# Performance work log

Hardware: AMD Instinct MI355X
Metric: run time of the kernel (lower is better)

Reference implementation:

```python
import jax, jax.numpy as jnp
import numpy as np

N_EMB = 512
DIM = 64
BETA = 0.25
EPS = 1e-10


def setup_inputs() -> dict:
    key = jax.random.key(0)
    k1, k2 = jax.random.split(key)
    z = jax.random.normal(k1, (32, 64, 64, 64), dtype=jnp.float32)  # (B, C=DIM, H, W)
    # embedding weight initialized uniform(-1/K, 1/K) as in the module
    weight = jax.random.uniform(k2, (N_EMB, DIM), dtype=jnp.float32,
                                minval=-1.0 / N_EMB, maxval=1.0 / N_EMB)
    return {"z": z, "weight": weight}


def reference(z, weight):
    # (B,C,H,W) -> (B,H,W,C)
    zp = jnp.transpose(z, (0, 2, 3, 1))
    zf = zp.reshape(-1, DIM)  # (N, D)
    # pairwise squared distances ||z||^2 + ||e||^2 - 2 z.e  -> (N, K)
    d = (jnp.sum(zf * zf, axis=1, keepdims=True)
         + jnp.sum(weight * weight, axis=1)
         - 2.0 * zf @ weight.T)
    codebook = jnp.argmin(d, axis=1)  # (N,)
    encodings = jax.nn.one_hot(codebook, N_EMB, dtype=zf.dtype)  # (N, K)
    # direct gather == one_hot @ weight (same math, efficient form)
    z_q = weight[codebook].reshape(zp.shape)
    sg = jax.lax.stop_gradient
    loss = jnp.mean((sg(z_q) - zp) ** 2) + BETA * jnp.mean((z_q - sg(zp)) ** 2)
    # straight-through estimator
    z_q = zp + sg(z_q - zp)
    e_mean = jnp.mean(encodings, axis=0)
    perplexity = jnp.exp(-jnp.sum(e_mean * jnp.log(e_mean + EPS)))
    z_q = jnp.transpose(z_q, (0, 3, 1, 2))  # back to (B,C,H,W)
    return (loss, z_q, perplexity, encodings, codebook)
```

## Files before the change

### kernel.cpp

```cpp
#include <hip/hip_runtime.h>
#include <math.h>

#define NK 512
#define NPTS (32*64*64)
#define NELEM (32*64*64*64)

#define OFF_LOSS 0
#define OFF_ZQ   1
#define OFF_PERP (1 + NELEM)
#define OFF_ENC  (2 + NELEM)
#define OFF_CB   (2 + NELEM + (size_t)NPTS * NK)


__global__ __launch_bounds__(256) void vq_prep(const float* __restrict__ wg,
                                               float* __restrict__ wT,
                                               float* __restrict__ bnd) {
    __shared__ float tl[64 * 65];
    const int t = threadIdx.x;
    const int kbase = blockIdx.x * 64;
    #pragma unroll
    for (int it = 0; it < 16; ++it) {
        int i = it * 256 + t;
        int k = i >> 6, d = i & 63;
        tl[k * 65 + d] = wg[(size_t)(kbase + k) * 64 + d];
    }
    __syncthreads();
    #pragma unroll
    for (int it = 0; it < 16; ++it) {
        int j = it * 256 + t;
        int d = j >> 6, kk = j & 63;
        wT[(size_t)d * 512 + kbase + kk] = tl[kk * 65 + d];
    }
    if (t < 64) {
        float s = 0.f;
        #pragma unroll 4
        for (int d = 0; d < 64; ++d) {
            float v = tl[t * 65 + d];
            s = __fadd_rn(s, __fmul_rn(v, v));
        }
        bnd[kbase + t] = s;
    }
}

__global__ __launch_bounds__(256, 2) void vq_main(const float* __restrict__ zg,
                                                  const float* __restrict__ wg,
                                                  const float* __restrict__ wT,
                                                  const float* __restrict__ bndg,
                                                  float* __restrict__ out,
                                                  int* __restrict__ hist,
                                                  double* __restrict__ lossAcc) {
    const int t = threadIdx.x;
    const int blk = blockIdx.x;
    const int b = blk >> 6;
    const int h = blk & 63;

    __shared__ __align__(16) float zt[64 * 64];
    __shared__ __align__(16) float wt[64 * 256];

    float* aRow = wt;
    float* redv = wt;
    int*   redi = (int*)(wt + 2048);
    float* zqt  = wt + 4096;
    int*   idxs = (int*)(wt + 8192);
    float* wsum = wt + 8256;

    {
        const int w = t & 63;
        const int c0 = t >> 6;
        const size_t base = (size_t)b * 262144 + (size_t)h * 64;
        #pragma unroll
        for (int c = c0; c < 64; c += 4)
            zt[c * 64 + w] = zg[base + (size_t)c * 4096 + w];
    }
    __syncthreads();

    if (t < 64) {
        float s = 0.f;
        for (int d = 0; d < 64; ++d) {
            float v = zt[d * 64 + t];
            s = __fadd_rn(s, __fmul_rn(v, v));
        }
        aRow[t] = s;
    }
    __syncthreads();

    const int tx = t & 7;
    const int ty = t >> 3;
    const int p0 = tx * 8;
    const int k0 = ty * 8;

    float av[8];
    {
        float4 a0 = *(const float4*)(aRow + p0);
        float4 a1 = *(const float4*)(aRow + p0 + 4);
        av[0] = a0.x; av[1] = a0.y; av[2] = a0.z; av[3] = a0.w;
        av[4] = a1.x; av[5] = a1.y; av[6] = a1.z; av[7] = a1.w;
    }
    __syncthreads();

    float best[8];
    int bidx[8];
    #pragma unroll
    for (int i = 0; i < 8; ++i) { best[i] = INFINITY; bidx[i] = 0; }

    const float4* wT4 = (const float4*)wT;
    float4* wt4 = (float4*)wt;

    for (int c = 0; c < 2; ++c) {
        if (c) __syncthreads();

        #pragma unroll
        for (int it = 0; it < 16; ++it) {
            int i = it * 256 + t;
            int d = i >> 6, c4 = i & 63;
            wt4[d * 64 + c4] = wT4[(size_t)d * 128 + c * 64 + c4];
        }

        float bn[8];
        {
            const float4* bp = (const float4*)(bndg + c * 256 + k0);
            float4 b0 = bp[0], b1 = bp[1];
            bn[0] = b0.x; bn[1] = b0.y; bn[2] = b0.z; bn[3] = b0.w;
            bn[4] = b1.x; bn[5] = b1.y; bn[6] = b1.z; bn[7] = b1.w;
        }
        __syncthreads();

        float acc[8][8];
        #pragma unroll
        for (int i = 0; i < 8; ++i)
            #pragma unroll
            for (int j = 0; j < 8; ++j) acc[i][j] = 0.f;

        const float* ztp = zt + p0;
        const float* wtp = wt + k0;
        #pragma unroll 4
        for (int d = 0; d < 64; ++d) {
            float4 z0 = *(const float4*)(ztp + d * 64);
            float4 z1 = *(const float4*)(ztp + d * 64 + 4);
            float4 w0 = *(const float4*)(wtp + d * 256);
            float4 w1 = *(const float4*)(wtp + d * 256 + 4);
            const float zr[8] = {z0.x, z0.y, z0.z, z0.w, z1.x, z1.y, z1.z, z1.w};
            const float wr[8] = {w0.x, w0.y, w0.z, w0.w, w1.x, w1.y, w1.z, w1.w};
            #pragma unroll
            for (int i = 0; i < 8; ++i)
                #pragma unroll
                for (int j = 0; j < 8; ++j)
                    acc[i][j] = fmaf(zr[i], wr[j], acc[i][j]);
        }

        #pragma unroll
        for (int i = 0; i < 8; ++i) {
            #pragma unroll
            for (int j = 0; j < 8; ++j) {
                float dist = __fsub_rn(__fadd_rn(av[i], bn[j]), 2.0f * acc[i][j]);
                int k = c * 256 + k0 + j;
                if (dist < best[i]) { best[i] = dist; bidx[i] = k; }
            }
        }
    }
    __syncthreads();

    #pragma unroll
    for (int i = 0; i < 8; ++i) {
        redv[ty * 64 + p0 + i] = best[i];
        redi[ty * 64 + p0 + i] = bidx[i];
    }
    __syncthreads();

    if (t < 64) {
        float bv = redv[t];
        int bi = redi[t];
        #pragma unroll
        for (int x = 1; x < 32; ++x) {
            float v = redv[x * 64 + t];
            int ii = redi[x * 64 + t];
            if (v < bv || (v == bv && ii < bi)) { bv = v; bi = ii; }
        }
        idxs[t] = bi;
        atomicAdd(&hist[bi], 1);
        out[OFF_CB + (size_t)blk * 64 + t] = (float)bi;
        const float4* wr4 = (const float4*)(wg + (size_t)bi * 64);
        #pragma unroll
        for (int q = 0; q < 16; ++q) {
            float4 v = wr4[q];
            zqt[(4 * q + 0) * 64 + t] = v.x;
            zqt[(4 * q + 1) * 64 + t] = v.y;
            zqt[(4 * q + 2) * 64 + t] = v.z;
            zqt[(4 * q + 3) * 64 + t] = v.w;
        }
    }
    __syncthreads();

    {
        float4* enc = (float4*)(out + OFF_ENC + (size_t)blk * 64 * NK);
        #pragma unroll
        for (int it = 0; it < 32; ++it) {
            int e = it * 256 + t;
            int r = e >> 7, cc = e & 127;
            int idx = idxs[r];
            float4 v = make_float4(0.f, 0.f, 0.f, 0.f);
            if ((idx >> 2) == cc) ((float*)&v)[idx & 3] = 1.0f;
            enc[(size_t)r * 128 + cc] = v;
        }
    }

    float lsum = 0.f;
    {
        float* zq = out + OFF_ZQ + (size_t)b * 262144 + (size_t)h * 64;
        #pragma unroll
        for (int it = 0; it < 4; ++it) {
            int f = it * 256 + t;
            int d = f >> 4, pp = (f & 15) * 4;
            float4 zv = *(const float4*)(zt + d * 64 + pp);
            float4 qv = *(const float4*)(zqt + d * 64 + pp);
            float4 o;
            float dx = __fsub_rn(qv.x, zv.x); lsum = __fadd_rn(lsum, __fmul_rn(dx, dx)); o.x = __fadd_rn(zv.x, dx);
            float dy = __fsub_rn(qv.y, zv.y); lsum = __fadd_rn(lsum, __fmul_rn(dy, dy)); o.y = __fadd_rn(zv.y, dy);
            float dz = __fsub_rn(qv.z, zv.z); lsum = __fadd_rn(lsum, __fmul_rn(dz, dz)); o.z = __fadd_rn(zv.z, dz);
            float dw = __fsub_rn(qv.w, zv.w); lsum = __fadd_rn(lsum, __fmul_rn(dw, dw)); o.w = __fadd_rn(zv.w, dw);
            *(float4*)(zq + (size_t)d * 4096 + pp) = o;
        }
    }
    #pragma unroll
    for (int off = 32; off > 0; off >>= 1)
        lsum += __shfl_down(lsum, off);
    if ((t & 63) == 0) wsum[t >> 6] = lsum;
    __syncthreads();
    if (t == 0) {
        float tot = (wsum[0] + wsum[1]) + (wsum[2] + wsum[3]);
        atomicAdd(lossAcc, (double)tot);
    }
}

__global__ __launch_bounds__(512) void vq_finalize(const int* __restrict__ hist,
                                                   const double* __restrict__ lossAcc,
                                                   float* __restrict__ out) {
    __shared__ float sh[512];
    const int t = threadIdx.x;
    float p = (float)hist[t] / (float)NPTS;
    sh[t] = __fmul_rn(p, logf(__fadd_rn(p, 1e-10f)));
    __syncthreads();
    for (int s = 256; s > 0; s >>= 1) {
        if (t < s) sh[t] += sh[t + s];
        __syncthreads();
    }
    if (t == 0) {
        float m = (float)(*lossAcc / (double)NELEM);
        out[OFF_LOSS] = __fadd_rn(m, __fmul_rn(0.25f, m));
        out[OFF_PERP] = expf(-sh[0]);
    }
}

extern "C" void kernel_launch(void* const* d_in, const int* in_sizes, int n_in,
                              void* d_out, int out_size, void* d_ws, size_t ws_size,
                              hipStream_t stream) {
    const float* z = (const float*)d_in[0];
    const float* w = (const float*)d_in[1];
    float* out = (float*)d_out;
    int* hist = (int*)d_ws;
    double* lossAcc = (double*)((char*)d_ws + 2048);
    float* wT = (float*)((char*)d_ws + 4096);
    float* bnd = wT + 64 * 512;

    (void)hipMemsetAsync(d_ws, 0, 4096, stream);
    vq_prep<<<8, 256, 0, stream>>>(w, wT, bnd);
    vq_main<<<2048, 256, 0, stream>>>(z, w, wT, bnd, out, hist, lossAcc);
    vq_finalize<<<1, 512, 0, stream>>>(hist, lossAcc, out);
}
```

Measured before the change: 463.0 us.

## Read codebook directly from global, shrink LDS, use nontemporal stores

Drops the shared-memory staging of the transposed codebook and reads weights straight from global/L2 inside the distance loop. This shrinks LDS use so occupancy can rise (launch bounds 2→4). The one-hot encodings and z_q outputs are now written with nontemporal stores to avoid cache pollution. The argmin reduction is split into two stages, and the codebook row gather is spread over 128 threads. In exchange, the inner loop now issues global loads instead of LDS reads, which may add latency.

```diff
diff --git a/kernel.cpp b/kernel.cpp
--- a/kernel.cpp
+++ b/kernel.cpp
@@ -10,6 +10,8 @@
 #define OFF_PERP (1 + NELEM)
 #define OFF_ENC  (2 + NELEM)
 #define OFF_CB   (2 + NELEM + (size_t)NPTS * NK)
+
+typedef float nt4 __attribute__((ext_vector_type(4)));
 
 
 __global__ __launch_bounds__(256) void vq_prep(const float* __restrict__ wg,
@@ -42,7 +44,7 @@
     }
 }
 
-__global__ __launch_bounds__(256, 2) void vq_main(const float* __restrict__ zg,
+__global__ __launch_bounds__(256, 4) void vq_main(const float* __restrict__ zg,
                                                   const float* __restrict__ wg,
                                                   const float* __restrict__ wT,
                                                   const float* __restrict__ bndg,
@@ -55,22 +57,26 @@
     const int h = blk & 63;
 
     __shared__ __align__(16) float zt[64 * 64];
-    __shared__ __align__(16) float wt[64 * 256];
-
-    float* aRow = wt;
-    float* redv = wt;
-    int*   redi = (int*)(wt + 2048);
-    float* zqt  = wt + 4096;
-    int*   idxs = (int*)(wt + 8192);
-    float* wsum = wt + 8256;
-
-    {
-        const int w = t & 63;
-        const int c0 = t >> 6;
+    __shared__ __align__(16) float buf[4096];
+    __shared__ __align__(16) float r2v[256];
+    __shared__ int   r2i[256];
+    __shared__ float aRow[64];
+    __shared__ int   idxs[64];
+    __shared__ float wsum[4];
+
+    float* redv = buf;
+    int*   redi = (int*)(buf + 2048);
+    float* zqt  = buf;
+
+    {
         const size_t base = (size_t)b * 262144 + (size_t)h * 64;
-        #pragma unroll
-        for (int c = c0; c < 64; c += 4)
-            zt[c * 64 + w] = zg[base + (size_t)c * 4096 + w];
+        const int w2 = (t & 31) * 2;
+        const int c0 = t >> 5;
+        #pragma unroll
+        for (int c = c0; c < 64; c += 8) {
+            float2 v = *(const float2*)(zg + base + (size_t)c * 4096 + w2);
+            *(float2*)(zt + c * 64 + w2) = v;
+        }
     }
     __syncthreads();
 
@@ -89,56 +95,29 @@
     const int p0 = tx * 8;
     const int k0 = ty * 8;
 
-    float av[8];
-    {
-        float4 a0 = *(const float4*)(aRow + p0);
-        float4 a1 = *(const float4*)(aRow + p0 + 4);
-        av[0] = a0.x; av[1] = a0.y; av[2] = a0.z; av[3] = a0.w;
-        av[4] = a1.x; av[5] = a1.y; av[6] = a1.z; av[7] = a1.w;
-    }
-    __syncthreads();
-
     float best[8];
     int bidx[8];
     #pragma unroll
     for (int i = 0; i < 8; ++i) { best[i] = INFINITY; bidx[i] = 0; }
 
-    const float4* wT4 = (const float4*)wT;
-    float4* wt4 = (float4*)wt;
-
+    const float* ztp = zt + p0;
+
+    #pragma unroll
     for (int c = 0; c < 2; ++c) {
-        if (c) __syncthreads();
-
-        #pragma unroll
-        for (int it = 0; it < 16; ++it) {
-            int i = it * 256 + t;
-            int d = i >> 6, c4 = i & 63;
-            wt4[d * 64 + c4] = wT4[(size_t)d * 128 + c * 64 + c4];
-        }
-
-        float bn[8];
-        {
-            const float4* bp = (const float4*)(bndg + c * 256 + k0);
-            float4 b0 = bp[0], b1 = bp[1];
-            bn[0] = b0.x; bn[1] = b0.y; bn[2] = b0.z; bn[3] = b0.w;
-            bn[4] = b1.x; bn[5] = b1.y; bn[6] = b1.z; bn[7] = b1.w;
-        }
-        __syncthreads();
-
         float acc[8][8];
         #pragma unroll
         for (int i = 0; i < 8; ++i)
             #pragma unroll
             for (int j = 0; j < 8; ++j) acc[i][j] = 0.f;
 
-        const float* ztp = zt + p0;
-        const float* wtp = wt + k0;
+        const float* wrow = wT + c * 256 + k0;
+
         #pragma unroll 4
         for (int d = 0; d < 64; ++d) {
             float4 z0 = *(const float4*)(ztp + d * 64);
             float4 z1 = *(const float4*)(ztp + d * 64 + 4);
-            float4 w0 = *(const float4*)(wtp + d * 256);
-            float4 w1 = *(const float4*)(wtp + d * 256 + 4);
+            float4 w0 = *(const float4*)(wrow + d * 512);
+            float4 w1 = *(const float4*)(wrow + d * 512 + 4);
             const float zr[8] = {z0.x, z0.y, z0.z, z0.w, z1.x, z1.y, z1.z, z1.w};
             const float wr[8] = {w0.x, w0.y, w0.z, w0.w, w1.x, w1.y, w1.z, w1.w};
             #pragma unroll
@@ -148,6 +127,21 @@
                     acc[i][j] = fmaf(zr[i], wr[j], acc[i][j]);
         }
 
+        float bn[8];
+        {
+            const float4* bp = (const float4*)(bndg + c * 256 + k0);
+            float4 b0 = bp[0], b1 = bp[1];
+            bn[0] = b0.x; bn[1] = b0.y; bn[2] = b0.z; bn[3] = b0.w;
+            bn[4] = b1.x; bn[5] = b1.y; bn[6] = b1.z; bn[7] = b1.w;
+        }
+        float av[8];
+        {
+            float4 a0 = *(const float4*)(aRow + p0);
+            float4 a1 = *(const float4*)(aRow + p0 + 4);
+            av[0] = a0.x; av[1] = a0.y; av[2] = a0.z; av[3] = a0.w;
+            av[4] = a1.x; av[5] = a1.y; av[6] = a1.z; av[7] = a1.w;
+        }
+
         #pragma unroll
         for (int i = 0; i < 8; ++i) {
             #pragma unroll
@@ -158,7 +152,6 @@
             }
         }
     }
-    __syncthreads();
 
     #pragma unroll
     for (int i = 0; i < 8; ++i) {
@@ -167,42 +160,63 @@
     }
     __syncthreads();
 
+    {
+        const int p = t & 63, g = t >> 6;
+        float bv = INFINITY; int bi = 0;
+        #pragma unroll
+        for (int x = g * 8; x < g * 8 + 8; ++x) {
+            float v = redv[x * 64 + p];
+            int ii = redi[x * 64 + p];
+            if (v < bv || (v == bv && ii < bi)) { bv = v; bi = ii; }
+        }
+        r2v[g * 64 + p] = bv;
+        r2i[g * 64 + p] = bi;
+    }
+    __syncthreads();
+
     if (t < 64) {
-        float bv = redv[t];
-        int bi = redi[t];
-        #pragma unroll
-        for (int x = 1; x < 32; ++x) {
-            float v = redv[x * 64 + t];
-            int ii = redi[x * 64 + t];
+        float bv = r2v[t];
+        int bi = r2i[t];
+        #pragma unroll
+        for (int g = 1; g < 4; ++g) {
+            float v = r2v[g * 64 + t];
+            int ii = r2i[g * 64 + t];
             if (v < bv || (v == bv && ii < bi)) { bv = v; bi = ii; }
         }
         idxs[t] = bi;
         atomicAdd(&hist[bi], 1);
         out[OFF_CB + (size_t)blk * 64 + t] = (float)bi;
-        const float4* wr4 = (const float4*)(wg + (size_t)bi * 64);
-        #pragma unroll
-        for (int q = 0; q < 16; ++q) {
+    }
+    __syncthreads();
+
+    if (t < 128) {
+        const int p = t >> 1, half = t & 1;
+        const int bi = idxs[p];
+        const float4* wr4 = (const float4*)(wg + (size_t)bi * 64) + half * 8;
+        #pragma unroll
+        for (int q = 0; q < 8; ++q) {
             float4 v = wr4[q];
-            zqt[(4 * q + 0) * 64 + t] = v.x;
-            zqt[(4 * q + 1) * 64 + t] = v.y;
-            zqt[(4 * q + 2) * 64 + t] = v.z;
-            zqt[(4 * q + 3) * 64 + t] = v.w;
-        }
-    }
-    __syncthreads();
-
-    {
-        float4* enc = (float4*)(out + OFF_ENC + (size_t)blk * 64 * NK);
+            int d = half * 32 + q * 4;
+            zqt[(d + 0) * 64 + p] = v.x;
+            zqt[(d + 1) * 64 + p] = v.y;
+            zqt[(d + 2) * 64 + p] = v.z;
+            zqt[(d + 3) * 64 + p] = v.w;
+        }
+    }
+
+    {
+        nt4* enc = (nt4*)(out + OFF_ENC + (size_t)blk * 64 * NK);
         #pragma unroll
         for (int it = 0; it < 32; ++it) {
             int e = it * 256 + t;
             int r = e >> 7, cc = e & 127;
             int idx = idxs[r];
-            float4 v = make_float4(0.f, 0.f, 0.f, 0.f);
-            if ((idx >> 2) == cc) ((float*)&v)[idx & 3] = 1.0f;
-            enc[(size_t)r * 128 + cc] = v;
-        }
-    }
+            nt4 v = {0.f, 0.f, 0.f, 0.f};
+            if ((idx >> 2) == cc) v[idx & 3] = 1.0f;
+            __builtin_nontemporal_store(v, &enc[(size_t)r * 128 + cc]);
+        }
+    }
+    __syncthreads();
 
     float lsum = 0.f;
     {
@@ -213,12 +227,12 @@
             int d = f >> 4, pp = (f & 15) * 4;
             float4 zv = *(const float4*)(zt + d * 64 + pp);
             float4 qv = *(const float4*)(zqt + d * 64 + pp);
-            float4 o;
+            nt4 o;
             float dx = __fsub_rn(qv.x, zv.x); lsum = __fadd_rn(lsum, __fmul_rn(dx, dx)); o.x = __fadd_rn(zv.x, dx);
             float dy = __fsub_rn(qv.y, zv.y); lsum = __fadd_rn(lsum, __fmul_rn(dy, dy)); o.y = __fadd_rn(zv.y, dy);
             float dz = __fsub_rn(qv.z, zv.z); lsum = __fadd_rn(lsum, __fmul_rn(dz, dz)); o.z = __fadd_rn(zv.z, dz);
             float dw = __fsub_rn(qv.w, zv.w); lsum = __fadd_rn(lsum, __fmul_rn(dw, dw)); o.w = __fadd_rn(zv.w, dw);
-            *(float4*)(zq + (size_t)d * 4096 + pp) = o;
+            __builtin_nontemporal_store(o, (nt4*)(zq + (size_t)d * 4096 + pp));
         }
     }
     #pragma unroll
```

New measurement: 472.9 us. 1.02x slower.
